# Kernel tuning notes

Hardware: AMD Instinct MI355X
Metric: run time of the kernel (lower is better)

The kernel has to match this reference:

```python
import jax, jax.numpy as jnp
import numpy as np
from jax.ops import segment_sum

N_NODES = 100000


def _add_self_loops(edge_index, n):
    loop = jnp.arange(n, dtype=edge_index.dtype)
    src = jnp.concatenate([edge_index[0], loop])
    dst = jnp.concatenate([edge_index[1], loop])
    return src, dst


def _gcn_conv(x, W, b, src, dst, n):
    # PyG GCNConv: h = X W; out[i] = sum_j norm(j,i) h[j] + b, with self-loops
    h = x @ W                                             # [N, out]
    deg = segment_sum(jnp.ones_like(src, dtype=x.dtype), dst, num_segments=n)
    dinv = jnp.where(deg > 0, jax.lax.rsqrt(deg), 0.0)    # deg^{-1/2}
    norm = dinv[src] * dinv[dst]                          # [E]
    msg = h[src] * norm[:, None]                          # gather + scale
    out = segment_sum(msg, dst, num_segments=n)           # scatter-add
    return out + b


def setup_inputs() -> dict:
    key = jax.random.key(0)
    ks = jax.random.split(key, 8)
    x = jax.random.normal(ks[0], (N_NODES, 128), dtype=jnp.float32)
    edge_index = jax.random.randint(ks[1], (2, 600000), 0, N_NODES, dtype=jnp.int64)
    s1 = 1.0 / np.sqrt(128); s2 = 1.0 / np.sqrt(64); s3 = 1.0 / np.sqrt(32)
    return {
        "x": x,
        "edge_index": edge_index,
        "W1": jax.random.uniform(ks[2], (128, 64), jnp.float32, -s1, s1),
        "b1": jnp.zeros((64,), jnp.float32),
        "W2": jax.random.uniform(ks[3], (64, 32), jnp.float32, -s2, s2),
        "b2": jnp.zeros((32,), jnp.float32),
        "Wc": jax.random.uniform(ks[4], (32, 1), jnp.float32, -s3, s3),
        "bc": jnp.zeros((1,), jnp.float32),
    }


def reference(x, edge_index, W1, b1, W2, b2, Wc, bc):
    n = x.shape[0]
    src, dst = _add_self_loops(edge_index, n)
    h = jax.nn.relu(_gcn_conv(x, W1, b1, src, dst, n))
    h = jax.nn.relu(_gcn_conv(h, W2, b2, src, dst, n))
    return h @ Wc + bc
```

## Files before the change

kernel.cpp:

```cpp
#include <hip/hip_runtime.h>


#define SCAN_THREADS 256
#define SCAN_PER_T   8
#define SCAN_TILE    (SCAN_THREADS * SCAN_PER_T)

__global__ __launch_bounds__(256) void count_kernel(const int* __restrict__ dst,
                                                    int* __restrict__ deg, int E) {
    int e = blockIdx.x * blockDim.x + threadIdx.x;
    if (e < E) atomicAdd(&deg[dst[e]], 1);
}

__global__ __launch_bounds__(SCAN_THREADS) void tile_reduce_kernel(const int* __restrict__ deg,
                                                                   int* __restrict__ bsum,
                                                                   int n) {
    __shared__ int s[SCAN_THREADS];
    int t = threadIdx.x;
    int gbase = blockIdx.x * SCAN_TILE + t * SCAN_PER_T;
    int local = 0;
#pragma unroll
    for (int k = 0; k < SCAN_PER_T; ++k) {
        int i = gbase + k;
        if (i < n) local += deg[i];
    }
    s[t] = local;
    __syncthreads();
    for (int off = SCAN_THREADS / 2; off > 0; off >>= 1) {
        if (t < off) s[t] += s[t + off];
        __syncthreads();
    }
    if (t == 0) bsum[blockIdx.x] = s[0];
}

__global__ __launch_bounds__(SCAN_THREADS) void scan_bsums_kernel(int* __restrict__ bsum,
                                                                  int* __restrict__ row_ptr,
                                                                  int nb, int n) {
    __shared__ int s[SCAN_THREADS];
    int t = threadIdx.x;
    s[t] = (t < nb) ? bsum[t] : 0;
    __syncthreads();
    for (int off = 1; off < SCAN_THREADS; off <<= 1) {
        int v = (t >= off) ? s[t - off] : 0;
        __syncthreads();
        s[t] += v;
        __syncthreads();
    }
    if (t < nb) bsum[t] = (t == 0) ? 0 : s[t - 1];
    if (t == 0) row_ptr[n] = s[nb - 1];
}

__global__ __launch_bounds__(SCAN_THREADS) void tile_apply_kernel(int* __restrict__ deg,
                                                                  const int* __restrict__ bsum,
                                                                  int* __restrict__ row_ptr,
                                                                  float* __restrict__ dinv,
                                                                  int n) {
    __shared__ int s[SCAN_THREADS];
    int t = threadIdx.x;
    int gbase = blockIdx.x * SCAN_TILE + t * SCAN_PER_T;

    int d[SCAN_PER_T];
    int inc[SCAN_PER_T];
    int run = 0;
#pragma unroll
    for (int k = 0; k < SCAN_PER_T; ++k) {
        int i = gbase + k;
        d[k] = (i < n) ? deg[i] : 0;
        run += d[k];
        inc[k] = run;
    }
    s[t] = run;
    __syncthreads();
    for (int off = 1; off < SCAN_THREADS; off <<= 1) {
        int v = (t >= off) ? s[t - off] : 0;
        __syncthreads();
        s[t] += v;
        __syncthreads();
    }
    int base = bsum[blockIdx.x] + ((t == 0) ? 0 : s[t - 1]);
#pragma unroll
    for (int k = 0; k < SCAN_PER_T; ++k) {
        int i = gbase + k;
        if (i < n) {
            int ex = base + inc[k] - d[k];
            row_ptr[i] = ex;
            deg[i] = ex;
            dinv[i] = rsqrtf((float)(d[k] + 1));
        }
    }
}

__global__ __launch_bounds__(256) void fill_kernel(const int* __restrict__ src,
                                                   const int* __restrict__ dst,
                                                   int* __restrict__ cursor,
                                                   int* __restrict__ col, int E) {
    int e = blockIdx.x * blockDim.x + threadIdx.x;
    if (e < E) {
        int pos = atomicAdd(&cursor[dst[e]], 1);
        col[pos] = src[e];
    }
}

template <int IN, int OUT, int BM, int TM, int TN>
__global__ __launch_bounds__(256) void gemm_tiled(const float* __restrict__ X,
                                                  const float* __restrict__ W,
                                                  float* __restrict__ H, int n) {
    constexpr int BK = 32;
    constexpr int S = 132;
    constexpr int NTX = OUT / TN;
    constexpr int NKT = IN / BK;
    static_assert(NTX * (BM / TM) == 256, "thread mapping");

    __shared__ float Ws[IN * OUT];
    __shared__ float Xs[2][BK * S];

    const int t = threadIdx.x;
    for (int i = t; i < IN * OUT / 4; i += 256)
        ((float4*)Ws)[i] = ((const float4*)W)[i];

    const int node0 = blockIdx.x * BM;
    const int tx = t % NTX;
    const int ty = t / NTX;
    const int row0 = ty * TM;
    const int jb = tx * TN;

    const int snd = t >> 3;
    const int skq = t & 7;

    float acc[TM][TN];
#pragma unroll
    for (int i = 0; i < TM; ++i)
#pragma unroll
        for (int j = 0; j < TN; ++j) acc[i][j] = 0.f;

    float4 stg[4];
#pragma unroll
    for (int i = 0; i < 4; ++i) {
        int nd = snd + 32 * i;
        stg[i] = make_float4(0.f, 0.f, 0.f, 0.f);
        if (node0 + nd < n)
            stg[i] = *(const float4*)(X + (size_t)(node0 + nd) * IN + skq * 4);
    }

    int cur = 0;
    for (int kt = 0; kt < NKT; ++kt) {
#pragma unroll
        for (int i = 0; i < 4; ++i) {
            int nd = snd + 32 * i;
            float* p = Xs[cur] + (skq * 4) * S + nd;
            p[0 * S] = stg[i].x;
            p[1 * S] = stg[i].y;
            p[2 * S] = stg[i].z;
            p[3 * S] = stg[i].w;
        }
        __syncthreads();

        if (kt + 1 < NKT) {
#pragma unroll
            for (int i = 0; i < 4; ++i) {
                int nd = snd + 32 * i;
                stg[i] = make_float4(0.f, 0.f, 0.f, 0.f);
                if (node0 + nd < n)
                    stg[i] = *(const float4*)(X + (size_t)(node0 + nd) * IN +
                                              (kt + 1) * BK + skq * 4);
            }
        }

        const float* xb = Xs[cur];
        const float* wb = Ws + (size_t)kt * BK * OUT + jb;
#pragma unroll 4
        for (int k = 0; k < BK; ++k) {
            float4 wv = *(const float4*)(wb + (size_t)k * OUT);
            float xv[TM];
#pragma unroll
            for (int i4 = 0; i4 < TM; i4 += 4) {
                float4 xq = *(const float4*)(xb + k * S + row0 + i4);
                xv[i4 + 0] = xq.x; xv[i4 + 1] = xq.y;
                xv[i4 + 2] = xq.z; xv[i4 + 3] = xq.w;
            }
#pragma unroll
            for (int i = 0; i < TM; ++i) {
                acc[i][0] += xv[i] * wv.x;
                acc[i][1] += xv[i] * wv.y;
                acc[i][2] += xv[i] * wv.z;
                acc[i][3] += xv[i] * wv.w;
            }
        }
        __syncthreads();
        cur ^= 1;
    }

#pragma unroll
    for (int i = 0; i < TM; ++i) {
        int node = node0 + row0 + i;
        if (node < n)
            *(float4*)(H + (size_t)node * OUT + jb) =
                make_float4(acc[i][0], acc[i][1], acc[i][2], acc[i][3]);
    }
}

template <int F>
__global__ __launch_bounds__(256) void agg_relu_kernel(const int* __restrict__ row_ptr,
                                                       const int* __restrict__ col,
                                                       const float* __restrict__ dinv,
                                                       const float* __restrict__ H,
                                                       const float* __restrict__ b,
                                                       float* __restrict__ OUT, int n) {
    constexpr int TPE = F / 4;
    int t = blockIdx.x * blockDim.x + threadIdx.x;
    int node = t / TPE;
    int c = t % TPE;
    if (node >= n) return;
    int rs = row_ptr[node], re = row_ptr[node + 1];
    float di = dinv[node];
    float4 acc = make_float4(0.f, 0.f, 0.f, 0.f);
    int e = rs;
    for (; e + 1 < re; e += 2) {
        int s0 = col[e], s1 = col[e + 1];
        float w0 = dinv[s0], w1 = dinv[s1];
        float4 v0 = *(const float4*)(H + (size_t)s0 * F + c * 4);
        float4 v1 = *(const float4*)(H + (size_t)s1 * F + c * 4);
        acc.x += w0 * v0.x + w1 * v1.x;
        acc.y += w0 * v0.y + w1 * v1.y;
        acc.z += w0 * v0.z + w1 * v1.z;
        acc.w += w0 * v0.w + w1 * v1.w;
    }
    if (e < re) {
        int s0 = col[e];
        float w0 = dinv[s0];
        float4 v0 = *(const float4*)(H + (size_t)s0 * F + c * 4);
        acc.x += w0 * v0.x; acc.y += w0 * v0.y;
        acc.z += w0 * v0.z; acc.w += w0 * v0.w;
    }
    float4 hs = *(const float4*)(H + (size_t)node * F + c * 4);
    float4 bb = *(const float4*)(b + c * 4);
    float d2 = di * di;
    float4 r;
    r.x = di * acc.x + d2 * hs.x + bb.x;
    r.y = di * acc.y + d2 * hs.y + bb.y;
    r.z = di * acc.z + d2 * hs.z + bb.z;
    r.w = di * acc.w + d2 * hs.w + bb.w;
    r.x = r.x > 0.f ? r.x : 0.f;
    r.y = r.y > 0.f ? r.y : 0.f;
    r.z = r.z > 0.f ? r.z : 0.f;
    r.w = r.w > 0.f ? r.w : 0.f;
    *(float4*)(OUT + (size_t)node * F + c * 4) = r;
}

__global__ __launch_bounds__(256) void agg_final_kernel(const int* __restrict__ row_ptr,
                                                        const int* __restrict__ col,
                                                        const float* __restrict__ dinv,
                                                        const float* __restrict__ H,
                                                        const float* __restrict__ b2,
                                                        const float* __restrict__ Wc,
                                                        const float* __restrict__ bc,
                                                        float* __restrict__ out, int n) {
    constexpr int F = 32, TPE = 8;
    int t = blockIdx.x * blockDim.x + threadIdx.x;
    int node = t / TPE;
    int c = t % TPE;
    if (node >= n) return;
    int rs = row_ptr[node], re = row_ptr[node + 1];
    float di = dinv[node];
    float4 acc = make_float4(0.f, 0.f, 0.f, 0.f);
    int e = rs;
    for (; e + 1 < re; e += 2) {
        int s0 = col[e], s1 = col[e + 1];
        float w0 = dinv[s0], w1 = dinv[s1];
        float4 v0 = *(const float4*)(H + (size_t)s0 * F + c * 4);
        float4 v1 = *(const float4*)(H + (size_t)s1 * F + c * 4);
        acc.x += w0 * v0.x + w1 * v1.x;
        acc.y += w0 * v0.y + w1 * v1.y;
        acc.z += w0 * v0.z + w1 * v1.z;
        acc.w += w0 * v0.w + w1 * v1.w;
    }
    if (e < re) {
        int s0 = col[e];
        float w0 = dinv[s0];
        float4 v0 = *(const float4*)(H + (size_t)s0 * F + c * 4);
        acc.x += w0 * v0.x; acc.y += w0 * v0.y;
        acc.z += w0 * v0.z; acc.w += w0 * v0.w;
    }
    float4 hs = *(const float4*)(H + (size_t)node * F + c * 4);
    float4 bb = *(const float4*)(b2 + c * 4);
    float4 wc = *(const float4*)(Wc + c * 4);
    float d2 = di * di;
    float4 r;
    r.x = di * acc.x + d2 * hs.x + bb.x;
    r.y = di * acc.y + d2 * hs.y + bb.y;
    r.z = di * acc.z + d2 * hs.z + bb.z;
    r.w = di * acc.w + d2 * hs.w + bb.w;
    float dot = (r.x > 0.f ? r.x : 0.f) * wc.x + (r.y > 0.f ? r.y : 0.f) * wc.y +
                (r.z > 0.f ? r.z : 0.f) * wc.z + (r.w > 0.f ? r.w : 0.f) * wc.w;
    dot += __shfl_xor(dot, 1, 8);
    dot += __shfl_xor(dot, 2, 8);
    dot += __shfl_xor(dot, 4, 8);
    if (c == 0) out[node] = dot + bc[0];
}

extern "C" void kernel_launch(void* const* d_in, const int* in_sizes, int n_in,
                              void* d_out, int out_size, void* d_ws, size_t ws_size,
                              hipStream_t stream) {
    const float* x  = (const float*)d_in[0];
    const int*   ei = (const int*)d_in[1];
    const float* W1 = (const float*)d_in[2];
    const float* b1 = (const float*)d_in[3];
    const float* W2 = (const float*)d_in[4];
    const float* b2 = (const float*)d_in[5];
    const float* Wc = (const float*)d_in[6];
    const float* bc = (const float*)d_in[7];
    float* out = (float*)d_out;

    const int n = in_sizes[0] / 128;
    const int E = in_sizes[1] / 2;

    const int* src = ei;
    const int* dst = ei + (size_t)E;

    const int nb = (n + SCAN_TILE - 1) / SCAN_TILE;

    float* dinv    = (float*)d_ws;
    int*   deg     = (int*)d_ws + n;
    int*   row_ptr = (int*)d_ws + 2 * (size_t)n;
    int*   col     = row_ptr + (n + 1);
    int*   bsum    = col + E;
    float* bufA    = (float*)(bsum + 256);
    float* bufB    = bufA + (size_t)n * 64;

    hipMemsetAsync(deg, 0, (size_t)n * 4, stream);
    count_kernel<<<(E + 255) / 256, 256, 0, stream>>>(dst, deg, E);
    tile_reduce_kernel<<<nb, SCAN_THREADS, 0, stream>>>(deg, bsum, n);
    scan_bsums_kernel<<<1, SCAN_THREADS, 0, stream>>>(bsum, row_ptr, nb, n);
    tile_apply_kernel<<<nb, SCAN_THREADS, 0, stream>>>(deg, bsum, row_ptr, dinv, n);
    fill_kernel<<<(E + 255) / 256, 256, 0, stream>>>(src, dst, deg, col, E);

    const int gemm_grid = (n + 127) / 128;

    gemm_tiled<128, 64, 128, 8, 4><<<gemm_grid, 256, 0, stream>>>(x, W1, bufA, n);
    agg_relu_kernel<64><<<(n * 16 + 255) / 256, 256, 0, stream>>>(row_ptr, col, dinv,
                                                                  bufA, b1, bufB, n);
    gemm_tiled<64, 32, 128, 4, 4><<<gemm_grid, 256, 0, stream>>>(bufB, W2, bufA, n);
    agg_final_kernel<<<(n * 8 + 255) / 256, 256, 0, stream>>>(row_ptr, col, dinv,
                                                              bufA, b2, Wc, bc, out, n);
}
```

Before: 267.0 us.

## Fold source-side deg^-1/2 into GEMM epilogue and unroll aggregation gathers

The GEMM epilogue now multiplies each output row by dinv[node], so H already holds dinv-scaled features. The aggregation kernels then drop the per-edge dinv[src] gather and multiply, sum neighbor rows directly, and apply dinv[dst] once at the end. The gather loop is unrolled to four edges so more loads are in flight, and the GEMM prefetches X two K-tiles ahead instead of one. The cost is more live registers in both kernels and a small change in floating-point rounding order.

```diff
diff --git a/kernel.cpp b/kernel.cpp
--- a/kernel.cpp
+++ b/kernel.cpp
@@ -103,6 +103,7 @@
 template <int IN, int OUT, int BM, int TM, int TN>
 __global__ __launch_bounds__(256) void gemm_tiled(const float* __restrict__ X,
                                                   const float* __restrict__ W,
+                                                  const float* __restrict__ dinv,
                                                   float* __restrict__ H, int n) {
     constexpr int BK = 32;
     constexpr int S = 132;
@@ -132,13 +133,22 @@
 #pragma unroll
         for (int j = 0; j < TN; ++j) acc[i][j] = 0.f;
 
-    float4 stg[4];
+    float4 stgA[4], stgB[4];
 #pragma unroll
     for (int i = 0; i < 4; ++i) {
         int nd = snd + 32 * i;
-        stg[i] = make_float4(0.f, 0.f, 0.f, 0.f);
+        stgA[i] = make_float4(0.f, 0.f, 0.f, 0.f);
         if (node0 + nd < n)
-            stg[i] = *(const float4*)(X + (size_t)(node0 + nd) * IN + skq * 4);
+            stgA[i] = *(const float4*)(X + (size_t)(node0 + nd) * IN + skq * 4);
+    }
+    if (NKT > 1) {
+#pragma unroll
+        for (int i = 0; i < 4; ++i) {
+            int nd = snd + 32 * i;
+            stgB[i] = make_float4(0.f, 0.f, 0.f, 0.f);
+            if (node0 + nd < n)
+                stgB[i] = *(const float4*)(X + (size_t)(node0 + nd) * IN + BK + skq * 4);
+        }
     }
 
     int cur = 0;
@@ -147,21 +157,20 @@
         for (int i = 0; i < 4; ++i) {
             int nd = snd + 32 * i;
             float* p = Xs[cur] + (skq * 4) * S + nd;
-            p[0 * S] = stg[i].x;
-            p[1 * S] = stg[i].y;
-            p[2 * S] = stg[i].z;
-            p[3 * S] = stg[i].w;
-        }
-        __syncthreads();
-
-        if (kt + 1 < NKT) {
+            float4 v = (kt & 1) ? stgB[i] : stgA[i];
+            p[0 * S] = v.x; p[1 * S] = v.y; p[2 * S] = v.z; p[3 * S] = v.w;
+        }
+        __syncthreads();
+
+        if (kt + 2 < NKT) {
 #pragma unroll
             for (int i = 0; i < 4; ++i) {
                 int nd = snd + 32 * i;
-                stg[i] = make_float4(0.f, 0.f, 0.f, 0.f);
+                float4 v = make_float4(0.f, 0.f, 0.f, 0.f);
                 if (node0 + nd < n)
-                    stg[i] = *(const float4*)(X + (size_t)(node0 + nd) * IN +
-                                              (kt + 1) * BK + skq * 4);
+                    v = *(const float4*)(X + (size_t)(node0 + nd) * IN +
+                                         (kt + 2) * BK + skq * 4);
+                if (kt & 1) stgB[i] = v; else stgA[i] = v;
             }
         }
 
@@ -192,9 +201,12 @@
 #pragma unroll
     for (int i = 0; i < TM; ++i) {
         int node = node0 + row0 + i;
-        if (node < n)
+        if (node < n) {
+            float di = dinv[node];
             *(float4*)(H + (size_t)node * OUT + jb) =
-                make_float4(acc[i][0], acc[i][1], acc[i][2], acc[i][3]);
+                make_float4(di * acc[i][0], di * acc[i][1],
+                            di * acc[i][2], di * acc[i][3]);
+        }
     }
 }
 
@@ -211,34 +223,32 @@
     int c = t % TPE;
     if (node >= n) return;
     int rs = row_ptr[node], re = row_ptr[node + 1];
-    float di = dinv[node];
     float4 acc = make_float4(0.f, 0.f, 0.f, 0.f);
     int e = rs;
-    for (; e + 1 < re; e += 2) {
-        int s0 = col[e], s1 = col[e + 1];
-        float w0 = dinv[s0], w1 = dinv[s1];
+    for (; e + 3 < re; e += 4) {
+        int s0 = col[e], s1 = col[e + 1], s2 = col[e + 2], s3 = col[e + 3];
         float4 v0 = *(const float4*)(H + (size_t)s0 * F + c * 4);
         float4 v1 = *(const float4*)(H + (size_t)s1 * F + c * 4);
-        acc.x += w0 * v0.x + w1 * v1.x;
-        acc.y += w0 * v0.y + w1 * v1.y;
-        acc.z += w0 * v0.z + w1 * v1.z;
-        acc.w += w0 * v0.w + w1 * v1.w;
-    }
-    if (e < re) {
+        float4 v2 = *(const float4*)(H + (size_t)s2 * F + c * 4);
+        float4 v3 = *(const float4*)(H + (size_t)s3 * F + c * 4);
+        acc.x += (v0.x + v1.x) + (v2.x + v3.x);
+        acc.y += (v0.y + v1.y) + (v2.y + v3.y);
+        acc.z += (v0.z + v1.z) + (v2.z + v3.z);
+        acc.w += (v0.w + v1.w) + (v2.w + v3.w);
+    }
+    for (; e < re; ++e) {
         int s0 = col[e];
-        float w0 = dinv[s0];
         float4 v0 = *(const float4*)(H + (size_t)s0 * F + c * 4);
-        acc.x += w0 * v0.x; acc.y += w0 * v0.y;
-        acc.z += w0 * v0.z; acc.w += w0 * v0.w;
-    }
+        acc.x += v0.x; acc.y += v0.y; acc.z += v0.z; acc.w += v0.w;
+    }
+    float di = dinv[node];
     float4 hs = *(const float4*)(H + (size_t)node * F + c * 4);
     float4 bb = *(const float4*)(b + c * 4);
-    float d2 = di * di;
     float4 r;
-    r.x = di * acc.x + d2 * hs.x + bb.x;
-    r.y = di * acc.y + d2 * hs.y + bb.y;
-    r.z = di * acc.z + d2 * hs.z + bb.z;
-    r.w = di * acc.w + d2 * hs.w + bb.w;
+    r.x = di * (acc.x + hs.x) + bb.x;
+    r.y = di * (acc.y + hs.y) + bb.y;
+    r.z = di * (acc.z + hs.z) + bb.z;
+    r.w = di * (acc.w + hs.w) + bb.w;
     r.x = r.x > 0.f ? r.x : 0.f;
     r.y = r.y > 0.f ? r.y : 0.f;
     r.z = r.z > 0.f ? r.z : 0.f;
@@ -260,35 +270,33 @@
     int c = t % TPE;
     if (node >= n) return;
     int rs = row_ptr[node], re = row_ptr[node + 1];
-    float di = dinv[node];
     float4 acc = make_float4(0.f, 0.f, 0.f, 0.f);
     int e = rs;
-    for (; e + 1 < re; e += 2) {
-        int s0 = col[e], s1 = col[e + 1];
-        float w0 = dinv[s0], w1 = dinv[s1];
+    for (; e + 3 < re; e += 4) {
+        int s0 = col[e], s1 = col[e + 1], s2 = col[e + 2], s3 = col[e + 3];
         float4 v0 = *(const float4*)(H + (size_t)s0 * F + c * 4);
         float4 v1 = *(const float4*)(H + (size_t)s1 * F + c * 4);
-        acc.x += w0 * v0.x + w1 * v1.x;
-        acc.y += w0 * v0.y + w1 * v1.y;
-        acc.z += w0 * v0.z + w1 * v1.z;
-        acc.w += w0 * v0.w + w1 * v1.w;
-    }
-    if (e < re) {
+        float4 v2 = *(const float4*)(H + (size_t)s2 * F + c * 4);
+        float4 v3 = *(const float4*)(H + (size_t)s3 * F + c * 4);
+        acc.x += (v0.x + v1.x) + (v2.x + v3.x);
+        acc.y += (v0.y + v1.y) + (v2.y + v3.y);
+        acc.z += (v0.z + v1.z) + (v2.z + v3.z);
+        acc.w += (v0.w + v1.w) + (v2.w + v3.w);
+    }
+    for (; e < re; ++e) {
         int s0 = col[e];
-        float w0 = dinv[s0];
         float4 v0 = *(const float4*)(H + (size_t)s0 * F + c * 4);
-        acc.x += w0 * v0.x; acc.y += w0 * v0.y;
-        acc.z += w0 * v0.z; acc.w += w0 * v0.w;
-    }
+        acc.x += v0.x; acc.y += v0.y; acc.z += v0.z; acc.w += v0.w;
+    }
+    float di = dinv[node];
     float4 hs = *(const float4*)(H + (size_t)node * F + c * 4);
     float4 bb = *(const float4*)(b2 + c * 4);
     float4 wc = *(const float4*)(Wc + c * 4);
-    float d2 = di * di;
     float4 r;
-    r.x = di * acc.x + d2 * hs.x + bb.x;
-    r.y = di * acc.y + d2 * hs.y + bb.y;
-    r.z = di * acc.z + d2 * hs.z + bb.z;
-    r.w = di * acc.w + d2 * hs.w + bb.w;
+    r.x = di * (acc.x + hs.x) + bb.x;
+    r.y = di * (acc.y + hs.y) + bb.y;
+    r.z = di * (acc.z + hs.z) + bb.z;
+    r.w = di * (acc.w + hs.w) + bb.w;
     float dot = (r.x > 0.f ? r.x : 0.f) * wc.x + (r.y > 0.f ? r.y : 0.f) * wc.y +
                 (r.z > 0.f ? r.z : 0.f) * wc.z + (r.w > 0.f ? r.w : 0.f) * wc.w;
     dot += __shfl_xor(dot, 1, 8);
@@ -335,10 +343,10 @@
 
     const int gemm_grid = (n + 127) / 128;
 
-    gemm_tiled<128, 64, 128, 8, 4><<<gemm_grid, 256, 0, stream>>>(x, W1, bufA, n);
+    gemm_tiled<128, 64, 128, 8, 4><<<gemm_grid, 256, 0, stream>>>(x, W1, dinv, bufA, n);
     agg_relu_kernel<64><<<(n * 16 + 255) / 256, 256, 0, stream>>>(row_ptr, col, dinv,
                                                                   bufA, b1, bufB, n);
-    gemm_tiled<64, 32, 128, 4, 4><<<gemm_grid, 256, 0, stream>>>(bufB, W2, bufA, n);
+    gemm_tiled<64, 32, 128, 4, 4><<<gemm_grid, 256, 0, stream>>>(bufB, W2, dinv, bufA, n);
     agg_final_kernel<<<(n * 8 + 255) / 256, 256, 0, stream>>>(row_ptr, col, dinv,
                                                               bufA, b2, Wc, bc, out, n);
 }
```

Result: no change. 266.5 us (-0.2%).
